# Kernel optimization log

Measured on AMD Instinct MI355X. Metric: run time of the kernel, lower is better.

## Reference

```python
import jax, jax.numpy as jnp
import numpy as np

B, N, C, T = 2048, 512, 64, 128  # batch, codebook size, latent channels, latent time


def setup_inputs() -> dict:
    key = jax.random.key(0)
    k1, k2 = jax.random.split(key)
    y = jax.random.normal(k1, (B, C, T), dtype=jnp.float32)   # encoder latents
    m = jax.random.normal(k2, (N, C, T), dtype=jnp.float32)   # centroid means
    sd = jnp.ones((N, C, T), dtype=jnp.float32)               # centroid variances
    p = jnp.zeros((N,), dtype=jnp.float32) + 1e-6             # cluster counts
    return {"y": y, "m": m, "sd": sd, "p": p}


def reference(y, m, sd, p):
    # --- squared-distance argmin assignment (same math as (y-m)^2 summed over C,T) ---
    b = y.shape[0]
    yf = y.reshape(b, -1)                 # [B, D]
    mf = m.reshape(m.shape[0], -1)        # [N, D]
    d2 = (yf * yf).sum(-1)[:, None] + (mf * mf).sum(-1)[None, :] - 2.0 * (yf @ mf.T)
    assign = jnp.argmin(d2, axis=1)       # [B] int assignments

    # --- sequential, order-sensitive EMA scatter updates (faithful to python loop) ---
    def step(carry, inp):
        p_, m_, sd_ = carry
        yi, zi = inp
        p_ = p_.at[zi].add(1.0)
        mi = m_[zi] * 0.001 + yi * 0.999
        m_ = m_.at[zi].set(mi)
        sdi = (mi - yi) ** 2 * 0.001 + sd_[zi] * 0.999
        sd_ = sd_.at[zi].set(sdi)
        return (p_, m_, sd_), None

    (p, m, sd), _ = jax.lax.scan(step, (p, m, sd), (y, assign))
    return m, sd, p, assign
```

## Files before the change

kernel.cpp:

```cpp
#include <hip/hip_runtime.h>
#include <hip/hip_bf16.h>


#define Bb 2048
#define Nn 512
#define Dd 8192
#define MARGIN 12.0f
#define KC 8
#define KSTEPS 16
#define BK 64

typedef __attribute__((ext_vector_type(4))) float f32x4;
typedef __attribute__((ext_vector_type(8))) short s16x8;
typedef __attribute__((ext_vector_type(2))) unsigned u32x2;

__device__ inline unsigned pack2(float lo, float hi) {
    return __builtin_amdgcn_perm(__float_as_uint(hi), __float_as_uint(lo), 0x07060302u);
}

__device__ inline void st4bf(unsigned short* dst, const float4 v) {
    u32x2 x;
    x[0] = pack2(v.x, v.y);
    x[1] = pack2(v.z, v.w);
    *(u32x2*)dst = x;
}

__device__ inline void ema4(float4& mcv, float4& scv, const float4 yv) {
#define EMA_C(c) { mcv.c = mcv.c * 0.001f + yv.c * 0.999f; \
                   float d_ = mcv.c - yv.c;                 \
                   scv.c = d_ * d_ * 0.001f + scv.c * 0.999f; }
    EMA_C(x) EMA_C(y) EMA_C(z) EMA_C(w)
#undef EMA_C
}

__global__ __launch_bounds__(256) void m_norms(const float* __restrict__ M,
                                               float* __restrict__ mm) {
    int n = blockIdx.x, t = threadIdx.x;
    const float4* r = (const float4*)(M + (size_t)n * Dd);
    float s = 0.f;
#pragma unroll
    for (int u = 0; u < 8; u++) {
        float4 v = r[t + 256 * u];
        s += v.x * v.x + v.y * v.y + v.z * v.z + v.w * v.w;
    }
    __shared__ float red[256];
    red[t] = s;
    __syncthreads();
    for (int off = 128; off > 0; off >>= 1) {
        if (t < off) red[t] += red[t + off];
        __syncthreads();
    }
    if (t == 0) mm[n] = red[0];
}

__global__ __launch_bounds__(512, 4) void gemm_coarse(const float* __restrict__ Y,
                                                      const float* __restrict__ M,
                                                      float* __restrict__ part) {
    __shared__ __align__(16) unsigned short As[2][128 * BK];
    __shared__ __align__(16) unsigned short Bs[2][128 * BK];
    const int t = threadIdx.x;
    const int lane = t & 63;
    const int w = t >> 6;

    const int bid = blockIdx.x;
    const int kc = bid & 7;
    const int ct = (bid >> 3) & 3;
    const int rt = bid >> 5;

    const size_t ybase = (size_t)rt * 128 * Dd + (size_t)kc * (KSTEPS * BK);
    const size_t mbase = (size_t)ct * 128 * Dd + (size_t)kc * (KSTEPS * BK);

    const int rL = t >> 3;
    const int c8 = t & 7;
    const float* gA0 = Y + ybase + (size_t)rL * Dd + c8 * 4;
    const float* gB0 = M + mbase + (size_t)rL * Dd + c8 * 4;
    const int swz = rL & 7;
    const int dA0 = rL * BK + ((((c8 >> 1) + 0) ^ swz) << 3) + (c8 & 1) * 4;
    const int dA1 = rL * BK + ((((c8 >> 1) + 4) ^ swz) << 3) + (c8 & 1) * 4;

    const int wr0 = (w & 3) * 32, wc0 = (w >> 2) * 64;
    const int l15 = lane & 15, quad = lane >> 4;

    f32x4 acc[2][4];
#pragma unroll
    for (int i = 0; i < 2; i++)
#pragma unroll
        for (int j = 0; j < 4; j++) acc[i][j] = (f32x4)(0.0f);

    float4 rA00, rA01, rA10, rA11;
    float4 rB00, rB01, rB10, rB11;
    const size_t rowskip = (size_t)64 * Dd;

    auto loads = [&](int step) {
        const float* pa = gA0 + step * BK;
        const float* pb = gB0 + step * BK;
        rA00 = *(const float4*)pa;             rA01 = *(const float4*)(pa + 32);
        rA10 = *(const float4*)(pa + rowskip); rA11 = *(const float4*)(pa + rowskip + 32);
        rB00 = *(const float4*)pb;             rB01 = *(const float4*)(pb + 32);
        rB10 = *(const float4*)(pb + rowskip); rB11 = *(const float4*)(pb + rowskip + 32);
    };
    auto writes = [&](int buf) {
        st4bf(&As[buf][dA0],            rA00);
        st4bf(&As[buf][dA1],            rA01);
        st4bf(&As[buf][dA0 + 64 * BK],  rA10);
        st4bf(&As[buf][dA1 + 64 * BK],  rA11);
        st4bf(&Bs[buf][dA0],            rB00);
        st4bf(&Bs[buf][dA1],            rB01);
        st4bf(&Bs[buf][dA0 + 64 * BK],  rB10);
        st4bf(&Bs[buf][dA1 + 64 * BK],  rB11);
    };
    auto compute = [&](int buf) {
#pragma unroll
        for (int ks = 0; ks < 2; ks++) {
            s16x8 fa[2], fb[4];
#pragma unroll
            for (int ta = 0; ta < 2; ta++) {
                int row = wr0 + ta * 16 + l15;
                int blk = (ks * 4 + quad) ^ (row & 7);
                fa[ta] = *(const s16x8*)(&As[buf][row * BK + (blk << 3)]);
            }
#pragma unroll
            for (int tb = 0; tb < 4; tb++) {
                int row = wc0 + tb * 16 + l15;
                int blk = (ks * 4 + quad) ^ (row & 7);
                fb[tb] = *(const s16x8*)(&Bs[buf][row * BK + (blk << 3)]);
            }
#pragma unroll
            for (int i = 0; i < 2; i++)
#pragma unroll
                for (int j = 0; j < 4; j++)
                    acc[i][j] = __builtin_amdgcn_mfma_f32_16x16x32_bf16(fa[i], fb[j], acc[i][j], 0, 0, 0);
        }
    };

#define BARRIER() do {                                          \
        asm volatile("s_waitcnt lgkmcnt(0)" ::: "memory");      \
        __builtin_amdgcn_s_barrier();                           \
    } while (0)

    loads(0);
    writes(0);
    BARRIER();
    for (int step = 0; step < KSTEPS; step++) {
        const int buf = step & 1;
        if (step + 1 < KSTEPS) loads(step + 1);
        compute(buf);
        if (step + 1 < KSTEPS) writes(buf ^ 1);
        BARRIER();
    }
#undef BARRIER

    float* P = part + (size_t)kc * (Bb * Nn);
#pragma unroll
    for (int i = 0; i < 2; i++) {
        int rg = rt * 128 + wr0 + i * 16 + quad * 4;
#pragma unroll
        for (int j = 0; j < 4; j++) {
            int cg = ct * 128 + wc0 + j * 16 + l15;
#pragma unroll
            for (int r = 0; r < 4; r++)
                P[(size_t)(rg + r) * Nn + cg] = acc[i][j][r];
        }
    }
}

__global__ __launch_bounds__(256) void rescore(const float* __restrict__ Y,
                                               const float* __restrict__ M,
                                               const float* __restrict__ part,
                                               const float* __restrict__ mm,
                                               float* __restrict__ assignF) {
    __shared__ float redW[4];
    __shared__ int candList[Nn];
    __shared__ float candD2[Nn];
    __shared__ int candCnt;
    int b = blockIdx.x, t = threadIdx.x, lane = t & 63, w = t >> 6;
    if (t == 0) candCnt = 0;

    int c0 = t, c1 = t + 256;
    float dot0 = 0.f, dot1 = 0.f;
#pragma unroll
    for (int k = 0; k < KC; k++) {
        dot0 += part[(size_t)k * (Bb * Nn) + (size_t)b * Nn + c0];
        dot1 += part[(size_t)k * (Bb * Nn) + (size_t)b * Nn + c1];
    }
    float d0 = mm[c0] - 2.0f * dot0;
    float d1 = mm[c1] - 2.0f * dot1;

    float mn = fminf(d0, d1);
#pragma unroll
    for (int off = 32; off > 0; off >>= 1) mn = fminf(mn, __shfl_xor(mn, off));
    if (lane == 0) redW[w] = mn;
    __syncthreads();
    float thresh = fminf(fminf(redW[0], redW[1]), fminf(redW[2], redW[3])) + MARGIN;

    if (d0 <= thresh) candList[atomicAdd(&candCnt, 1)] = c0;
    if (d1 <= thresh) candList[atomicAdd(&candCnt, 1)] = c1;
    __syncthreads();
    int ncand = candCnt;

    if (ncand == 1) {
        if (t == 0) assignF[b] = (float)candList[0];
        return;
    }

    const float4* yr = (const float4*)(Y + (size_t)b * Dd);
    for (int j = w; j < ncand; j += 4) {
        int c = candList[j];
        const float4* mr = (const float4*)(M + (size_t)c * Dd);
        float p = 0.f;
#pragma unroll 8
        for (int u = 0; u < 32; u++) {
            float4 yv = yr[u * 64 + lane];
            float4 mv = mr[u * 64 + lane];
            p += yv.x * mv.x + yv.y * mv.y + yv.z * mv.z + yv.w * mv.w;
        }
#pragma unroll
        for (int off = 32; off > 0; off >>= 1) p += __shfl_xor(p, off);
        if (lane == 0) candD2[j] = mm[c] - 2.0f * p;
    }
    __syncthreads();

    if (t == 0) {
        float bestV = 3.4e38f;
        int bestI = 0x3fffffff;
        for (int j = 0; j < ncand; j++) {
            float d2e = candD2[j];
            int c = candList[j];
            if (d2e < bestV || (d2e == bestV && c < bestI)) { bestV = d2e; bestI = c; }
        }
        assignF[b] = (float)bestI;
    }
}

__global__ __launch_bounds__(256) void ema_scatter(const float* __restrict__ Y,
                                                   const float* __restrict__ M0,
                                                   const float* __restrict__ SD0,
                                                   const float* __restrict__ P0,
                                                   const float* __restrict__ assignF,
                                                   float* __restrict__ m_out,
                                                   float* __restrict__ sd_out,
                                                   float* __restrict__ p_out) {
    __shared__ int lst[Bb];
    __shared__ int cnt4[4];
    int n = blockIdx.x, s = blockIdx.y, t = threadIdx.x, lane = t & 63, w = t >> 6;

    int eqf[8], myidx[8];
    int cntW = 0;
#pragma unroll
    for (int k = 0; k < 8; k++) {
        int u = w * 8 + k;
        int zi = (int)assignF[u * 64 + lane];
        int eq = (zi == n) ? 1 : 0;
        unsigned long long mask = __ballot(eq != 0);
        eqf[k] = eq;
        myidx[k] = cntW + (int)__popcll(mask & ((1ull << lane) - 1ull));
        cntW += (int)__popcll(mask);
    }
    if (lane == 0) cnt4[w] = cntW;
    __syncthreads();
    int off0 = 0;
#pragma unroll
    for (int q = 0; q < 4; q++) off0 += (q < w) ? cnt4[q] : 0;
    int cnt = cnt4[0] + cnt4[1] + cnt4[2] + cnt4[3];
#pragma unroll
    for (int k = 0; k < 8; k++)
        if (eqf[k]) lst[off0 + myidx[k]] = (w * 8 + k) * 64 + lane;
    if (t == 0 && s == 0) p_out[n] = P0[n] + (float)cnt;
    __syncthreads();

    size_t off = (size_t)n * Dd + (size_t)s * 1024;
    float4 mc = *(const float4*)(M0 + off + 4 * t);
    float4 sc = *(const float4*)(SD0 + off + 4 * t);

    int j = 0;
    for (; j + 16 <= cnt; j += 16) {
        float4 yv[16];
#pragma unroll
        for (int q = 0; q < 16; q++)
            yv[q] = *(const float4*)(Y + (size_t)lst[j + q] * Dd + (size_t)s * 1024 + 4 * t);
#pragma unroll
        for (int q = 0; q < 16; q++) ema4(mc, sc, yv[q]);
    }
    for (; j + 4 <= cnt; j += 4) {
        float4 yv[4];
#pragma unroll
        for (int q = 0; q < 4; q++)
            yv[q] = *(const float4*)(Y + (size_t)lst[j + q] * Dd + (size_t)s * 1024 + 4 * t);
#pragma unroll
        for (int q = 0; q < 4; q++) ema4(mc, sc, yv[q]);
    }
    for (; j < cnt; j++) {
        float4 yv = *(const float4*)(Y + (size_t)lst[j] * Dd + (size_t)s * 1024 + 4 * t);
        ema4(mc, sc, yv);
    }

    *(float4*)(m_out + off + 4 * t) = mc;
    *(float4*)(sd_out + off + 4 * t) = sc;
}

extern "C" void kernel_launch(void* const* d_in, const int* in_sizes, int n_in,
                              void* d_out, int out_size, void* d_ws, size_t ws_size,
                              hipStream_t stream) {
    const float* y  = (const float*)d_in[0];
    const float* m  = (const float*)d_in[1];
    const float* sd = (const float*)d_in[2];
    const float* p  = (const float*)d_in[3];

    float* out     = (float*)d_out;
    float* m_out   = out;
    float* sd_out  = out + 4194304;
    float* p_out   = out + 8388608;
    float* assignF = out + 8389120;
    float* part    = out;

    m_norms    <<<Nn, 256, 0, stream>>>(m, p_out);
    gemm_coarse<<<dim3(512), 512, 0, stream>>>(y, m, part);
    rescore    <<<Bb, 256, 0, stream>>>(y, m, part, p_out, assignF);
    ema_scatter<<<dim3(Nn, 8), 256, 0, stream>>>(y, m, sd, p, assignF, m_out, sd_out, p_out);
}
```

Before: 212.3 us.

## Shrink coarse GEMM tiles to 64x64 with BK=32 and drop LDS swizzle

The coarse bf16 distance GEMM now uses 64x64 output tiles, a K-step of 32 and 256-thread blocks, launching 2048 blocks instead of 512. The aim is more blocks and higher occupancy, so latency hides better and the 256 CUs fill more evenly. In exchange each block reuses its loaded data less, so global/L2 traffic for Y and M roughly doubles, and it needs twice as many barriers. The XOR swizzle on the shared-memory layout is also removed, which may bring back LDS bank conflicts on the fragment reads.

```diff
diff --git a/kernel.cpp b/kernel.cpp
--- a/kernel.cpp
+++ b/kernel.cpp
@@ -7,8 +7,8 @@
 #define Dd 8192
 #define MARGIN 12.0f
 #define KC 8
-#define KSTEPS 16
-#define BK 64
+#define KSTEPS 32
+#define BK 32
 
 typedef __attribute__((ext_vector_type(4))) float f32x4;
 typedef __attribute__((ext_vector_type(8))) short s16x8;
@@ -53,84 +53,66 @@
     if (t == 0) mm[n] = red[0];
 }
 
-__global__ __launch_bounds__(512, 4) void gemm_coarse(const float* __restrict__ Y,
+__global__ __launch_bounds__(256, 8) void gemm_coarse(const float* __restrict__ Y,
                                                       const float* __restrict__ M,
                                                       float* __restrict__ part) {
-    __shared__ __align__(16) unsigned short As[2][128 * BK];
-    __shared__ __align__(16) unsigned short Bs[2][128 * BK];
+    __shared__ __align__(16) unsigned short As[2][64 * BK];
+    __shared__ __align__(16) unsigned short Bs[2][64 * BK];
     const int t = threadIdx.x;
     const int lane = t & 63;
     const int w = t >> 6;
 
     const int bid = blockIdx.x;
     const int kc = bid & 7;
-    const int ct = (bid >> 3) & 3;
-    const int rt = bid >> 5;
-
-    const size_t ybase = (size_t)rt * 128 * Dd + (size_t)kc * (KSTEPS * BK);
-    const size_t mbase = (size_t)ct * 128 * Dd + (size_t)kc * (KSTEPS * BK);
+    const int ct = (bid >> 3) & 7;
+    const int rt = bid >> 6;
+
+    const size_t ybase = (size_t)rt * 64 * Dd + (size_t)kc * (KSTEPS * BK);
+    const size_t mbase = (size_t)ct * 64 * Dd + (size_t)kc * (KSTEPS * BK);
 
     const int rL = t >> 3;
-    const int c8 = t & 7;
-    const float* gA0 = Y + ybase + (size_t)rL * Dd + c8 * 4;
-    const float* gB0 = M + mbase + (size_t)rL * Dd + c8 * 4;
-    const int swz = rL & 7;
-    const int dA0 = rL * BK + ((((c8 >> 1) + 0) ^ swz) << 3) + (c8 & 1) * 4;
-    const int dA1 = rL * BK + ((((c8 >> 1) + 4) ^ swz) << 3) + (c8 & 1) * 4;
-
-    const int wr0 = (w & 3) * 32, wc0 = (w >> 2) * 64;
+    const int c4 = (t & 7) * 4;
+    const float* gA0 = Y + ybase + (size_t)rL * Dd + c4;
+    const float* gB0 = M + mbase + (size_t)rL * Dd + c4;
+    const int dst0 = rL * BK + c4;
+    const size_t rowskip = (size_t)32 * Dd;
+
+    const int wr0 = (w & 1) * 32, wc0 = (w >> 1) * 32;
     const int l15 = lane & 15, quad = lane >> 4;
 
-    f32x4 acc[2][4];
+    f32x4 acc[2][2];
 #pragma unroll
     for (int i = 0; i < 2; i++)
 #pragma unroll
-        for (int j = 0; j < 4; j++) acc[i][j] = (f32x4)(0.0f);
-
-    float4 rA00, rA01, rA10, rA11;
-    float4 rB00, rB01, rB10, rB11;
-    const size_t rowskip = (size_t)64 * Dd;
+        for (int j = 0; j < 2; j++) acc[i][j] = (f32x4)(0.0f);
+
+    float4 rA0, rA1, rB0, rB1;
 
     auto loads = [&](int step) {
         const float* pa = gA0 + step * BK;
         const float* pb = gB0 + step * BK;
-        rA00 = *(const float4*)pa;             rA01 = *(const float4*)(pa + 32);
-        rA10 = *(const float4*)(pa + rowskip); rA11 = *(const float4*)(pa + rowskip + 32);
-        rB00 = *(const float4*)pb;             rB01 = *(const float4*)(pb + 32);
-        rB10 = *(const float4*)(pb + rowskip); rB11 = *(const float4*)(pb + rowskip + 32);
+        rA0 = *(const float4*)pa;  rA1 = *(const float4*)(pa + rowskip);
+        rB0 = *(const float4*)pb;  rB1 = *(const float4*)(pb + rowskip);
     };
     auto writes = [&](int buf) {
-        st4bf(&As[buf][dA0],            rA00);
-        st4bf(&As[buf][dA1],            rA01);
-        st4bf(&As[buf][dA0 + 64 * BK],  rA10);
-        st4bf(&As[buf][dA1 + 64 * BK],  rA11);
-        st4bf(&Bs[buf][dA0],            rB00);
-        st4bf(&Bs[buf][dA1],            rB01);
-        st4bf(&Bs[buf][dA0 + 64 * BK],  rB10);
-        st4bf(&Bs[buf][dA1 + 64 * BK],  rB11);
+        st4bf(&As[buf][dst0],        rA0);
+        st4bf(&As[buf][dst0 + 1024], rA1);
+        st4bf(&Bs[buf][dst0],        rB0);
+        st4bf(&Bs[buf][dst0 + 1024], rB1);
     };
     auto compute = [&](int buf) {
-#pragma unroll
-        for (int ks = 0; ks < 2; ks++) {
-            s16x8 fa[2], fb[4];
-#pragma unroll
-            for (int ta = 0; ta < 2; ta++) {
-                int row = wr0 + ta * 16 + l15;
-                int blk = (ks * 4 + quad) ^ (row & 7);
-                fa[ta] = *(const s16x8*)(&As[buf][row * BK + (blk << 3)]);
-            }
-#pragma unroll
-            for (int tb = 0; tb < 4; tb++) {
-                int row = wc0 + tb * 16 + l15;
-                int blk = (ks * 4 + quad) ^ (row & 7);
-                fb[tb] = *(const s16x8*)(&Bs[buf][row * BK + (blk << 3)]);
-            }
-#pragma unroll
-            for (int i = 0; i < 2; i++)
-#pragma unroll
-                for (int j = 0; j < 4; j++)
-                    acc[i][j] = __builtin_amdgcn_mfma_f32_16x16x32_bf16(fa[i], fb[j], acc[i][j], 0, 0, 0);
-        }
+        s16x8 fa[2], fb[2];
+#pragma unroll
+        for (int ta = 0; ta < 2; ta++)
+            fa[ta] = *(const s16x8*)(&As[buf][(wr0 + ta * 16 + l15) * BK + quad * 8]);
+#pragma unroll
+        for (int tb = 0; tb < 2; tb++)
+            fb[tb] = *(const s16x8*)(&Bs[buf][(wc0 + tb * 16 + l15) * BK + quad * 8]);
+#pragma unroll
+        for (int i = 0; i < 2; i++)
+#pragma unroll
+            for (int j = 0; j < 2; j++)
+                acc[i][j] = __builtin_amdgcn_mfma_f32_16x16x32_bf16(fa[i], fb[j], acc[i][j], 0, 0, 0);
     };
 
 #define BARRIER() do {                                          \
@@ -153,10 +135,10 @@
     float* P = part + (size_t)kc * (Bb * Nn);
 #pragma unroll
     for (int i = 0; i < 2; i++) {
-        int rg = rt * 128 + wr0 + i * 16 + quad * 4;
-#pragma unroll
-        for (int j = 0; j < 4; j++) {
-            int cg = ct * 128 + wc0 + j * 16 + l15;
+        int rg = rt * 64 + wr0 + i * 16 + quad * 4;
+#pragma unroll
+        for (int j = 0; j < 2; j++) {
+            int cg = ct * 64 + wc0 + j * 16 + l15;
 #pragma unroll
             for (int r = 0; r < 4; r++)
                 P[(size_t)(rg + r) * Nn + cg] = acc[i][j][r];
@@ -314,7 +296,7 @@
     float* part    = out;
 
     m_norms    <<<Nn, 256, 0, stream>>>(m, p_out);
-    gemm_coarse<<<dim3(512), 512, 0, stream>>>(y, m, part);
+    gemm_coarse<<<dim3(2048), 256, 0, stream>>>(y, m, part);
     rescore    <<<Bb, 256, 0, stream>>>(y, m, part, p_out, assignF);
     ema_scatter<<<dim3(Nn, 8), 256, 0, stream>>>(y, m, sd, p, assignF, m_out, sd_out, p_out);
 }
```

After: 234.6 us. 10.5% more time.
